# Kernel optimization log

Hardware: AMD Instinct MI355X
Metric: run time of the kernel (lower is better)

Reference implementation:

```python
import jax, jax.numpy as jnp
import numpy as np


def setup_inputs() -> dict:
    key = jax.random.key(0)
    ks = jax.random.split(key, 8)
    B, Cq, Ckv, Co, T, H, W = 2, 256, 256, 256, 8, 28, 28
    s = 1.0 / np.sqrt(Cq)
    return {
        "x": jax.random.normal(ks[0], (B, Cq, T, H, W), jnp.float32),
        "context": jax.random.normal(ks[1], (B, Ckv, T, H, W), jnp.float32),
        "wq": jax.random.normal(ks[2], (Co, Cq), jnp.float32) * s,
        "bq": jnp.zeros((Co,), jnp.float32),
        "wk": jax.random.normal(ks[3], (Co, Ckv), jnp.float32) * s,
        "bk": jnp.zeros((Co,), jnp.float32),
        "wv": jax.random.normal(ks[4], (Co, Ckv), jnp.float32) * s,
        "bv": jnp.zeros((Co,), jnp.float32),
    }


def reference(x, context, wq, bq, wk, bk, wv, bv):
    B, C, T, H, W = x.shape
    N = T * H * W
    Co = wq.shape[0]
    # 1x1x1 Conv3d == per-voxel linear projection over channels
    def proj(inp, w, b):
        y = jnp.einsum('bcthw,oc->bothw', inp, w) + b[None, :, None, None, None]
        return y.reshape(B, Co, N)  # [B, Co, N]
    q = proj(x, wq, bq).transpose(0, 2, 1)        # [B, N, Co]
    k = proj(context, wk, bk)                     # [B, Co, Nc]
    v = proj(context, wv, bv).transpose(0, 2, 1)  # [B, Nc, Co]
    scale = 1.0 / jnp.sqrt(jnp.asarray(Co, x.dtype))
    attn = jax.nn.softmax(jnp.einsum('bnc,bcm->bnm', q, k) * scale, axis=-1)
    out = jnp.einsum('bnm,bmc->bnc', attn, v)     # [B, N, Co]
    out = out.transpose(0, 2, 1).reshape(B, Co, T, H, W)
    return out + x
```

## Files before the change

### kernel.cpp

```cpp
#include <hip/hip_runtime.h>
#include <hip/hip_bf16.h>
#include <math.h>

#define BB 2
#define CC 256
#define NN 6272
#define NT16 392
#define NKB32 196
#define SCL 0.09016844005f

typedef __attribute__((ext_vector_type(8))) short s8v;
typedef __attribute__((ext_vector_type(4))) float f4v;

__device__ inline unsigned short f2bf(float f) {
  unsigned u = __builtin_bit_cast(unsigned, f);
  u += 0x7fffu + ((u >> 16) & 1u);
  return (unsigned short)(u >> 16);
}

__global__ __launch_bounds__(256) void wcvt_kernel(
    const float* __restrict__ wq, const float* __restrict__ wk,
    const float* __restrict__ wv, unsigned short* __restrict__ Wb)
{
  int i = (blockIdx.x * 256 + threadIdx.x) * 4;
  const float* src = (i < 65536) ? wq : (i < 131072 ? wk : wv);
  int off = i & 65535;
  float4 v = *(const float4*)(src + off);
  ushort4 o;
  o.x = f2bf(v.x); o.y = f2bf(v.y); o.z = f2bf(v.z); o.w = f2bf(v.w);
  *(ushort4*)(Wb + i) = o;
}

__global__ __launch_bounds__(256) void proj_kernel(
    const float* __restrict__ x, const float* __restrict__ ctx,
    const unsigned short* __restrict__ Wb,
    const float* __restrict__ bq, const float* __restrict__ bk,
    const float* __restrict__ bv,
    unsigned short* __restrict__ Q, unsigned short* __restrict__ Kk,
    unsigned short* __restrict__ V)
{
  const int p = blockIdx.z, b = blockIdx.y;
  const int n0 = blockIdx.x * 32;
  const int tid = threadIdx.x;
  const float* in = (p == 0 ? x : ctx) + (size_t)b * CC * NN;
  const unsigned short* W = Wb + (size_t)p * 65536;
  const float* bias = (p == 0 ? bq : (p == 1 ? bk : bv));

  __shared__ __align__(16) unsigned short lds[32][264];
  for (int it = tid; it < 2048; it += 256) {
    int c  = it >> 3;
    int n4 = (it & 7) << 2;
    float4 v = *(const float4*)(in + (size_t)c * NN + n0 + n4);
    lds[n4 + 0][c] = f2bf(v.x);
    lds[n4 + 1][c] = f2bf(v.y);
    lds[n4 + 2][c] = f2bf(v.z);
    lds[n4 + 3][c] = f2bf(v.w);
  }
  __syncthreads();

  const int lane = tid & 63, l15 = lane & 15, g = lane >> 4;
  const int obase = (tid >> 6) * 64;

  f4v acc[4][2];
#pragma unroll
  for (int mt = 0; mt < 4; ++mt) {
    float4 b4 = *(const float4*)(bias + obase + mt * 16 + g * 4);
    f4v bi = {b4.x, b4.y, b4.z, b4.w};
    acc[mt][0] = bi; acc[mt][1] = bi;
  }

#pragma unroll
  for (int ks = 0; ks < 8; ++ks) {
    s8v bf0 = *(const s8v*)(&lds[l15][ks * 32 + g * 8]);
    s8v bf1 = *(const s8v*)(&lds[16 + l15][ks * 32 + g * 8]);
#pragma unroll
    for (int mt = 0; mt < 4; ++mt) {
      s8v wa = *(const s8v*)(W + (size_t)(obase + mt * 16 + l15) * CC + ks * 32 + g * 8);
      acc[mt][0] = __builtin_amdgcn_mfma_f32_16x16x32_bf16(wa, bf0, acc[mt][0], 0, 0, 0);
      acc[mt][1] = __builtin_amdgcn_mfma_f32_16x16x32_bf16(wa, bf1, acc[mt][1], 0, 0, 0);
    }
  }

  if (p == 0) {
#pragma unroll
    for (int mt = 0; mt < 4; ++mt)
#pragma unroll
      for (int qq = 0; qq < 2; ++qq)
#pragma unroll
        for (int r = 0; r < 4; ++r)
          acc[mt][qq][r] *= SCL;
  }

  if (p < 2) {
    unsigned short* dst = (p == 0 ? Q : Kk) + (size_t)b * NN * CC;
#pragma unroll
    for (int mt = 0; mt < 4; ++mt)
#pragma unroll
      for (int qq = 0; qq < 2; ++qq) {
        ushort4 pk;
        pk.x = f2bf(acc[mt][qq][0]); pk.y = f2bf(acc[mt][qq][1]);
        pk.z = f2bf(acc[mt][qq][2]); pk.w = f2bf(acc[mt][qq][3]);
        *(ushort4*)(dst + (size_t)(n0 + qq * 16 + l15) * CC + obase + mt * 16 + g * 4) = pk;
      }
  } else {
    unsigned short* dstb = V + (size_t)b * CC * NN;
#pragma unroll
    for (int mt = 0; mt < 4; ++mt)
#pragma unroll
      for (int qq = 0; qq < 2; ++qq)
#pragma unroll
        for (int r = 0; r < 4; ++r)
          dstb[(size_t)(obase + mt * 16 + g * 4 + r) * NN + n0 + qq * 16 + l15] =
              f2bf(acc[mt][qq][r]);
  }
}

__global__ __launch_bounds__(512, 4) void attn_kernel(
    const unsigned short* __restrict__ Qg,
    const unsigned short* __restrict__ Kg,
    const unsigned short* __restrict__ Vg,
    float* __restrict__ Opart,
    float* __restrict__ ml,
    int split, int kb_base, int kb_rem)
{
  const int s     = blockIdx.x % split;
  const int stile = blockIdx.x / split;
  const int b     = stile / 49;
  const int qsup  = stile % 49;
  const int tid   = threadIdx.x;
  const int w     = tid >> 6;
  const int lane  = tid & 63;
  const int l15 = lane & 15, g = lane >> 4;
  const int qt16  = qsup * 8 + w;
  const int q0    = qt16 * 16;
  const int wid16 = b * NT16 + qt16;

  const int start = s * kb_base + (s < kb_rem ? s : kb_rem);
  const int cnt   = kb_base + (s < kb_rem ? 1 : 0);

  const unsigned short* Qb = Qg + (size_t)b * NN * CC;
  const unsigned short* Kb = Kg + (size_t)b * NN * CC;
  const unsigned short* Vb = Vg + (size_t)b * CC * NN;

  __shared__ __align__(16) unsigned short K_lds[2][32 * 256];
  __shared__ __align__(16) unsigned short V_lds[2][256 * 32];
  __shared__ __align__(16) unsigned short P_lds[8][16][36];

  s8v qf[8];
#pragma unroll
  for (int ks = 0; ks < 8; ++ks)
    qf[ks] = *(const s8v*)(Qb + (size_t)(q0 + l15) * CC + ks * 32 + g * 8);

  f4v ot[16];
  const f4v fz = {0.f, 0.f, 0.f, 0.f};
#pragma unroll
  for (int mt = 0; mt < 16; ++mt) ot[mt] = fz;

  float lsum = 0.f;

  auto stage = [&](int buf, int kb32) {
    const int kb = kb32 * 32;
#pragma unroll
    for (int i = 0; i < 4; ++i) {
      if (w < 4) {
        int chunk = w * 256 + i * 64 + lane;
        int r = chunk >> 5, cc = chunk & 31;
        const unsigned short* gp =
            Kb + (size_t)(kb + r) * CC + ((cc ^ (r & 15)) << 3);
        __builtin_amdgcn_global_load_lds(
            (const __attribute__((address_space(1))) unsigned int*)gp,
            (__attribute__((address_space(3))) unsigned int*)(&K_lds[buf][chunk * 8]),
            16, 0, 0);
      } else {
        int vc = (w - 4) * 256 + i * 64 + lane;
        int ch = vc >> 2, cc = vc & 3;
        const unsigned short* gp =
            Vb + (size_t)ch * NN + kb + ((cc ^ ((ch >> 1) & 3)) << 3);
        __builtin_amdgcn_global_load_lds(
            (const __attribute__((address_space(1))) unsigned int*)gp,
            (__attribute__((address_space(3))) unsigned int*)(&V_lds[buf][vc * 8]),
            16, 0, 0);
      }
    }
  };

  stage(0, start);
  int cur = 0;

  for (int ib = 0; ib < cnt; ++ib) {
    __syncthreads();
    if (ib + 1 < cnt) stage(cur ^ 1, start + ib + 1);

    const unsigned short* Kl = &K_lds[cur][0];
    const unsigned short* Vl = &V_lds[cur][0];

    f4v st[2];
    st[0] = fz; st[1] = fz;
#pragma unroll
    for (int ks = 0; ks < 8; ++ks) {
      const int co = ((ks * 4 + g) ^ l15) << 3;
#pragma unroll
      for (int kt = 0; kt < 2; ++kt) {
        s8v ka = *(const s8v*)(Kl + (kt * 16 + l15) * 256 + co);
        st[kt] = __builtin_amdgcn_mfma_f32_16x16x32_bf16(ka, qf[ks], st[kt], 0, 0, 0);
      }
    }

#pragma unroll
    for (int kt = 0; kt < 2; ++kt) {
      float p0 = __builtin_amdgcn_exp2f(st[kt][0]);
      float p1 = __builtin_amdgcn_exp2f(st[kt][1]);
      float p2 = __builtin_amdgcn_exp2f(st[kt][2]);
      float p3 = __builtin_amdgcn_exp2f(st[kt][3]);
      lsum += (p0 + p1) + (p2 + p3);
      ushort4 pk;
      pk.x = f2bf(p0); pk.y = f2bf(p1); pk.z = f2bf(p2); pk.w = f2bf(p3);
      *(ushort4*)(&P_lds[w][l15][kt * 16 + 4 * g]) = pk;
    }

    s8v pb = *(const s8v*)(&P_lds[w][l15][g * 8]);
    const int vo = (g ^ ((l15 >> 1) & 3)) << 3;
#pragma unroll
    for (int mt = 0; mt < 16; ++mt) {
      s8v va = *(const s8v*)(Vl + (mt * 16 + l15) * 32 + vo);
      ot[mt] = __builtin_amdgcn_mfma_f32_16x16x32_bf16(va, pb, ot[mt], 0, 0, 0);
    }

    cur ^= 1;
  }

  lsum += __shfl_xor(lsum, 16);
  lsum += __shfl_xor(lsum, 32);

  float* Ob = Opart + (size_t)(wid16 * split + s) * 4096;
#pragma unroll
  for (int mt = 0; mt < 16; ++mt)
    __builtin_nontemporal_store(ot[mt], (f4v*)(Ob + mt * 256 + lane * 4));

  if (lane < 16)
    ml[(size_t)(wid16 * split + s) * 16 + lane] = lsum;
}

__global__ __launch_bounds__(256) void merge_kernel(
    const float* __restrict__ Opart,
    const float* __restrict__ ml,
    const float* __restrict__ x,
    float* __restrict__ out,
    int split)
{
  const int wid16 = blockIdx.x;
  const int b  = wid16 / NT16;
  const int q0 = (wid16 % NT16) * 16;
  const int tid = threadIdx.x;
  const int w = tid >> 6;
  const int lane = tid & 63;
  const int l15 = lane & 15, g = lane >> 4;

  float L = 0.f;
#pragma unroll
  for (int s = 0; s < 8; ++s)
    if (s < split)
      L += ml[(size_t)(wid16 * split + s) * 16 + l15];
  const float invL = 1.f / L;

#pragma unroll
  for (int j = 0; j < 4; ++j) {
    int mt = j * 4 + w;
    f4v a = {0.f, 0.f, 0.f, 0.f};
#pragma unroll
    for (int s = 0; s < 8; ++s)
      if (s < split) {
        const f4v* Op4 = (const f4v*)(Opart + (size_t)(wid16 * split + s) * 4096);
        f4v o4 = __builtin_nontemporal_load(Op4 + mt * 64 + lane);
        a += o4;
      }
#pragma unroll
    for (int r = 0; r < 4; ++r) {
      int c = mt * 16 + g * 4 + r;
      size_t idx = ((size_t)b * CC + c) * NN + q0 + l15;
      out[idx] = a[r] * invL + x[idx];
    }
  }
}

extern "C" void kernel_launch(void* const* d_in, const int* in_sizes, int n_in,
                              void* d_out, int out_size, void* d_ws, size_t ws_size,
                              hipStream_t stream) {
  const float* x   = (const float*)d_in[0];
  const float* ctx = (const float*)d_in[1];
  const float* wq  = (const float*)d_in[2];
  const float* bq  = (const float*)d_in[3];
  const float* wk  = (const float*)d_in[4];
  const float* bk  = (const float*)d_in[5];
  const float* wv  = (const float*)d_in[6];
  const float* bv  = (const float*)d_in[7];
  float* out = (float*)d_out;

  const size_t sz = (size_t)BB * NN * CC;
  unsigned short* Wb = (unsigned short*)d_ws;
  unsigned short* Q  = Wb + 3 * 65536;
  unsigned short* K  = Q + sz;
  unsigned short* V  = K + sz;
  const size_t fixedB = 3 * 65536 * 2 + 3 * sz * 2;

  int split = 1;
  const int cands[3] = {5, 2, 1};
  for (int i = 0; i < 3; ++i) {
    size_t need = fixedB + (size_t)cands[i] * (BB * NT16) * (4096 + 16) * sizeof(float);
    if (ws_size >= need) { split = cands[i]; break; }
  }
  float* Opart = (float*)((char*)d_ws + fixedB);
  float* ml    = Opart + (size_t)split * (BB * NT16) * 4096;
  const int kb_base = NKB32 / split, kb_rem = NKB32 % split;

  wcvt_kernel<<<dim3(192), dim3(256), 0, stream>>>(wq, wk, wv, Wb);
  proj_kernel<<<dim3(NN / 32, BB, 3), dim3(256), 0, stream>>>(
      x, ctx, Wb, bq, bk, bv, Q, K, V);
  attn_kernel<<<dim3(98 * split), dim3(512), 0, stream>>>(
      Q, K, V, Opart, ml, split, kb_base, kb_rem);
  merge_kernel<<<dim3(BB * NT16), dim3(256), 0, stream>>>(Opart, ml, x, out, split);
}
```

Baseline: 267.2 us.

## Store split-attention partials in bf16 and transpose merge output via LDS

The attention kernel now writes its per-split unnormalized output partials as bf16 instead of fp32, halving the partial buffer that the merge kernel must read back. The merge kernel now handles 32 query positions per block and stages normalized results in padded shared memory, so the residual add and output store run along contiguous positions in 32-float rows. This cuts global memory traffic and improves store coalescing. The cost is bf16 rounding of the unnormalized partial sums before they are accumulated.

```diff
diff --git a/kernel.cpp b/kernel.cpp
--- a/kernel.cpp
+++ b/kernel.cpp
@@ -11,11 +11,17 @@
 
 typedef __attribute__((ext_vector_type(8))) short s8v;
 typedef __attribute__((ext_vector_type(4))) float f4v;
+typedef __attribute__((ext_vector_type(4))) unsigned short us4v;
 
 __device__ inline unsigned short f2bf(float f) {
   unsigned u = __builtin_bit_cast(unsigned, f);
   u += 0x7fffu + ((u >> 16) & 1u);
   return (unsigned short)(u >> 16);
+}
+
+__device__ inline float bf2f(unsigned short h) {
+  unsigned u = (unsigned)h << 16;
+  return __builtin_bit_cast(float, u);
 }
 
 __global__ __launch_bounds__(256) void wcvt_kernel(
@@ -119,7 +125,7 @@
     const unsigned short* __restrict__ Qg,
     const unsigned short* __restrict__ Kg,
     const unsigned short* __restrict__ Vg,
-    float* __restrict__ Opart,
+    unsigned short* __restrict__ Opart,
     float* __restrict__ ml,
     int split, int kb_base, int kb_rem)
 {
@@ -232,54 +238,77 @@
   lsum += __shfl_xor(lsum, 16);
   lsum += __shfl_xor(lsum, 32);
 
-  float* Ob = Opart + (size_t)(wid16 * split + s) * 4096;
-#pragma unroll
-  for (int mt = 0; mt < 16; ++mt)
-    __builtin_nontemporal_store(ot[mt], (f4v*)(Ob + mt * 256 + lane * 4));
+  unsigned short* Ob = Opart + (size_t)(wid16 * split + s) * 4096;
+#pragma unroll
+  for (int mt = 0; mt < 16; ++mt) {
+    us4v o4;
+    o4.x = f2bf(ot[mt][0]); o4.y = f2bf(ot[mt][1]);
+    o4.z = f2bf(ot[mt][2]); o4.w = f2bf(ot[mt][3]);
+    __builtin_nontemporal_store(o4, (us4v*)(Ob + mt * 256 + lane * 4));
+  }
 
   if (lane < 16)
     ml[(size_t)(wid16 * split + s) * 16 + lane] = lsum;
 }
 
 __global__ __launch_bounds__(256) void merge_kernel(
-    const float* __restrict__ Opart,
+    const unsigned short* __restrict__ Opart,
     const float* __restrict__ ml,
     const float* __restrict__ x,
     float* __restrict__ out,
     int split)
 {
-  const int wid16 = blockIdx.x;
-  const int b  = wid16 / NT16;
-  const int q0 = (wid16 % NT16) * 16;
+  const int wid32 = blockIdx.x;
+  const int b  = wid32 / (NT16 / 2);
+  const int pi = wid32 % (NT16 / 2);
+  const int n0 = pi * 32;
   const int tid = threadIdx.x;
   const int w = tid >> 6;
   const int lane = tid & 63;
   const int l15 = lane & 15, g = lane >> 4;
 
-  float L = 0.f;
-#pragma unroll
-  for (int s = 0; s < 8; ++s)
-    if (s < split)
-      L += ml[(size_t)(wid16 * split + s) * 16 + l15];
-  const float invL = 1.f / L;
-
-#pragma unroll
-  for (int j = 0; j < 4; ++j) {
-    int mt = j * 4 + w;
-    f4v a = {0.f, 0.f, 0.f, 0.f};
+  __shared__ float lds_o[256][33];
+
+#pragma unroll
+  for (int t = 0; t < 2; ++t) {
+    const int wid16 = b * NT16 + pi * 2 + t;
+    float L = 0.f;
 #pragma unroll
     for (int s = 0; s < 8; ++s)
-      if (s < split) {
-        const f4v* Op4 = (const f4v*)(Opart + (size_t)(wid16 * split + s) * 4096);
-        f4v o4 = __builtin_nontemporal_load(Op4 + mt * 64 + lane);
-        a += o4;
-      }
-#pragma unroll
-    for (int r = 0; r < 4; ++r) {
-      int c = mt * 16 + g * 4 + r;
-      size_t idx = ((size_t)b * CC + c) * NN + q0 + l15;
-      out[idx] = a[r] * invL + x[idx];
-    }
+      if (s < split)
+        L += ml[(size_t)(wid16 * split + s) * 16 + l15];
+    const float invL = 1.f / L;
+
+#pragma unroll
+    for (int j = 0; j < 4; ++j) {
+      int mt = j * 4 + w;
+      float a0 = 0.f, a1 = 0.f, a2 = 0.f, a3 = 0.f;
+#pragma unroll
+      for (int s = 0; s < 8; ++s)
+        if (s < split) {
+          const us4v* Op4 = (const us4v*)(Opart + (size_t)(wid16 * split + s) * 4096);
+          us4v o4 = __builtin_nontemporal_load(Op4 + mt * 64 + lane);
+          a0 += bf2f(o4.x); a1 += bf2f(o4.y);
+          a2 += bf2f(o4.z); a3 += bf2f(o4.w);
+        }
+      int c = mt * 16 + g * 4;
+      int nl = t * 16 + l15;
+      lds_o[c + 0][nl] = a0 * invL;
+      lds_o[c + 1][nl] = a1 * invL;
+      lds_o[c + 2][nl] = a2 * invL;
+      lds_o[c + 3][nl] = a3 * invL;
+    }
+  }
+  __syncthreads();
+
+  const size_t base = (size_t)b * CC * NN + n0;
+  const int n = tid & 31;
+  const int c0 = tid >> 5;
+#pragma unroll
+  for (int cg = 0; cg < 32; ++cg) {
+    int c = cg * 8 + c0;
+    size_t idx = base + (size_t)c * NN + n;
+    out[idx] = lds_o[c][n] + x[idx];
   }
 }
 
@@ -306,11 +335,12 @@
   int split = 1;
   const int cands[3] = {5, 2, 1};
   for (int i = 0; i < 3; ++i) {
-    size_t need = fixedB + (size_t)cands[i] * (BB * NT16) * (4096 + 16) * sizeof(float);
+    size_t need = fixedB + (size_t)cands[i] * (BB * NT16) *
+                  (4096 * sizeof(unsigned short) + 16 * sizeof(float));
     if (ws_size >= need) { split = cands[i]; break; }
   }
-  float* Opart = (float*)((char*)d_ws + fixedB);
-  float* ml    = Opart + (size_t)split * (BB * NT16) * 4096;
+  unsigned short* Opart = (unsigned short*)((char*)d_ws + fixedB);
+  float* ml = (float*)(Opart + (size_t)split * (BB * NT16) * 4096);
   const int kb_base = NKB32 / split, kb_rem = NKB32 % split;
 
   wcvt_kernel<<<dim3(192), dim3(256), 0, stream>>>(wq, wk, wv, Wb);
@@ -318,5 +348,6 @@
       x, ctx, Wb, bq, bk, bv, Q, K, V);
   attn_kernel<<<dim3(98 * split), dim3(512), 0, stream>>>(
       Q, K, V, Opart, ml, split, kb_base, kb_rem);
-  merge_kernel<<<dim3(BB * NT16), dim3(256), 0, stream>>>(Opart, ml, x, out, split);
-}
+  merge_kernel<<<dim3(BB * NT16 / 2), dim3(256), 0, stream>>>(
+      Opart, ml, x, out, split);
+}
```

Measured after the change: 293.8 us. +10.0%, slower.
